# Kernel optimization log

Hardware: AMD Instinct MI355X
Metric: run time of the kernel (lower is better)

The kernel has to match this reference:

```python
import jax, jax.numpy as jnp
import numpy as np

N, SEQ_LEN, HORIZON, F_IN, EMBED, HIDDEN, LAYERS = 4096, 168, 24, 32, 32, 64, 2
G4 = 4 * HIDDEN
# NOTE: original torch code calls nn.LSTM per-step WITHOUT carrying hidden state,
# so each step's LSTM starts from (h0=0, c0=0): W_hh contributes nothing, only b_hh.

def setup_inputs() -> dict:
    key = jax.random.key(0)
    ks = jax.random.split(key, 12)
    s = 0.1
    return {
        "X": jax.random.normal(ks[0], (N, SEQ_LEN, F_IN), jnp.float32),
        "y": jax.random.normal(ks[1], (N, SEQ_LEN), jnp.float32),
        "Xf": jax.random.normal(ks[2], (N, HORIZON, F_IN), jnp.float32),
        "W_embed": jax.random.normal(ks[3], (EMBED, 1), jnp.float32) * s,
        "b_embed": jax.random.normal(ks[4], (EMBED,), jnp.float32) * s,
        "W_ih": jax.random.normal(ks[5], (LAYERS, G4, EMBED + F_IN), jnp.float32) * s,  # layer1 in-dim == HIDDEN == EMBED+F_IN
        "b_ih": jax.random.normal(ks[6], (LAYERS, G4), jnp.float32) * s,
        "b_hh": jax.random.normal(ks[7], (LAYERS, G4), jnp.float32) * s,
        "W_mu": jax.random.normal(ks[8], (1, HIDDEN), jnp.float32) * s,
        "b_mu": jax.random.normal(ks[9], (1,), jnp.float32) * s,
        "W_sigma": jax.random.normal(ks[10], (1, HIDDEN), jnp.float32) * s,
        "b_sigma": jax.random.normal(ks[11], (1,), jnp.float32) * s,
    }


def reference(X, y, Xf, W_embed, b_embed, W_ih, b_ih, b_hh, W_mu, b_mu, W_sigma, b_sigma):
    num_ts = X.shape[0]
    T = SEQ_LEN + HORIZON
    Xall = jnp.concatenate([X, Xf], axis=1)  # (N, T, F_IN)
    y_pad = jnp.concatenate([y, jnp.zeros((num_ts, HORIZON), y.dtype)], axis=1)  # (N, T)
    use_y = jnp.arange(T) < SEQ_LEN  # teacher-forced region

    def step(carry, inputs):
        x_s, y_s, use = inputs  # (N, F_IN), (N,), scalar bool
        ynext = jnp.where(use, y_s[:, None], carry)  # (N, 1)
        yembed = ynext @ W_embed.T + b_embed  # (N, EMBED)
        h = jnp.concatenate([x_s, yembed], axis=1)  # (N, F_IN+EMBED)
        for l in range(LAYERS):  # single LSTM step from zero state per layer
            gates = h @ W_ih[l].T + b_ih[l] + b_hh[l]  # (N, 4H); torch gate order i,f,g,o
            i_g, f_g, g_g, o_g = jnp.split(gates, 4, axis=1)
            c = jax.nn.sigmoid(i_g) * jnp.tanh(g_g)  # f * c0 term vanishes (c0 = 0)
            h = jax.nn.sigmoid(o_g) * jnp.tanh(c)
        h = jax.nn.relu(h)
        mu = h @ W_mu.T + b_mu  # (N, 1)
        sigma = jax.nn.softplus(h @ W_sigma.T + b_sigma) + 1e-6  # log(1+exp(.)) + eps
        lik = (2.0 * np.pi * sigma ** 2) ** (-0.5) * jnp.exp(-((ynext - mu) ** 2) / (2.0 * sigma ** 2))
        return lik, (lik[:, 0], mu[:, 0], sigma[:, 0])

    carry0 = jnp.zeros((num_ts, 1), X.dtype)
    xs = (jnp.swapaxes(Xall, 0, 1), y_pad.T, use_y)
    _, (lik_t, mu_t, sigma_t) = jax.lax.scan(step, carry0, xs)  # each (T, N)
    ypred = lik_t.T[:, SEQ_LEN - 1: SEQ_LEN + HORIZON - 1]  # (N, HORIZON)
    return ypred, mu_t.T, sigma_t.T
```

## Files before the change

### kernel.cpp

```cpp
#include <hip/hip_runtime.h>
#include <math.h>

#define N_TS 4096
#define SEQ  168
#define HOR  24
#define T_ALL 192
#define F_INP 32
#define HID  64
#define NROW 192
#define NB_B (N_TS / 32)
#define NT_B ((N_TS * SEQ) / 128)
#define L2E  1.44269504089f
#define W16F_L1 6144

typedef _Float16 half8  __attribute__((ext_vector_type(8)));
typedef _Float16 half4  __attribute__((ext_vector_type(4)));
typedef float    floatx4 __attribute__((ext_vector_type(4)));

__device__ __forceinline__ float fexp(float x)  { return __expf(x); }
__device__ __forceinline__ float ex2(float x)   { return __builtin_amdgcn_exp2f(x); }
__device__ __forceinline__ float frcp(float x)  { return __builtin_amdgcn_rcpf(x); }
__device__ __forceinline__ float softplus_(float x) { return (x > 15.0f) ? x : __logf(1.0f + fexp(x)); }

__device__ __forceinline__ float lstm_h(float ip, float gp, float op) {
    const float Ei = ex2(ip);
    const float Eg = ex2(gp);
    const float cc = (1.0f - Eg) * frcp((1.0f + Ei) * (1.0f + Eg));
    const float Ec = ex2(cc * (-2.0f * L2E));
    const float Eo = ex2(op);
    return (1.0f - Ec) * frcp((1.0f + Ec) * (1.0f + Eo));
}

__device__ __forceinline__ half8 cvt8(const float4 a, const float4 b) {
    half8 v;
    v[0]=(_Float16)a.x; v[1]=(_Float16)a.y; v[2]=(_Float16)a.z; v[3]=(_Float16)a.w;
    v[4]=(_Float16)b.x; v[5]=(_Float16)b.y; v[6]=(_Float16)b.z; v[7]=(_Float16)b.w;
    return v;
}

__global__ __launch_bounds__(256) void prep(
    const float* __restrict__ W_ih, const float* __restrict__ b_ih,
    const float* __restrict__ b_hh,
    const float* __restrict__ W_embed, const float* __restrict__ b_embed,
    _Float16* __restrict__ W16f, float* __restrict__ bsum,
    float* __restrict__ wy1, float* __restrict__ b1c)
{
    const int idx = blockIdx.x * 256 + threadIdx.x;
    for (int i = idx; i < 4 * NROW * 8; i += gridDim.x * 256) {
        const int kp  = i & 7;
        const int row = (i >> 3) % NROW;
        const int kb  = (i >> 3) / NROW;
        const int sr  = (row < 64) ? row : row + 64;
        const float sc = (row >= 64 && row < 128) ? (-2.0f * L2E) : (-L2E);
        W16f[i] = (_Float16)(W_ih[sr * HID + kb * 8 + kp] * sc);
    }
    for (int i = idx; i < 8 * NROW * 8; i += gridDim.x * 256) {
        const int kp  = i & 7;
        const int row = (i >> 3) % NROW;
        const int kb  = (i >> 3) / NROW;
        const int sr  = (row < 64) ? row : row + 64;
        const float sc = (row >= 64 && row < 128) ? (-2.0f * L2E) : (-L2E);
        W16f[W16F_L1 + i] = (_Float16)(W_ih[(256 + sr) * HID + kb * 8 + kp] * sc);
    }
    for (int i = idx; i < 2 * NROW; i += gridDim.x * 256) {
        const int r = i % NROW;
        const int l = i / NROW;
        const int sr = (r < 64) ? r : r + 64;
        const float sc = (r >= 64 && r < 128) ? (-2.0f * L2E) : (-L2E);
        bsum[i] = (b_ih[l * 256 + sr] + b_hh[l * 256 + sr]) * sc;
    }
    if (idx < NROW) {
        const int sr = (idx < 64) ? idx : idx + 64;
        const float sc = (idx >= 64 && idx < 128) ? (-2.0f * L2E) : (-L2E);
        const float* wrow = W_ih + sr * HID + 32;
        float s1 = 0.f, s2 = 0.f;
        #pragma unroll
        for (int k = 0; k < 32; ++k) {
            s1 = fmaf(wrow[k], W_embed[k], s1);
            s2 = fmaf(wrow[k], b_embed[k], s2);
        }
        wy1[idx] = s1 * sc;
        b1c[idx] = (b_ih[sr] + b_hh[sr] + s2) * sc;
    }
}

__global__ __launch_bounds__(512, 8) void fused(
    const float* __restrict__ X,
    const float* __restrict__ y,
    const float* __restrict__ Xf,
    const float* __restrict__ W_embed,
    const float* __restrict__ b_embed,
    const _Float16* __restrict__ W16f,
    const float* __restrict__ bsum,
    const float* __restrict__ wy1,
    const float* __restrict__ b1c,
    const float* __restrict__ W_mu,
    const float* __restrict__ b_mu,
    const float* __restrict__ W_sigma,
    const float* __restrict__ b_sigma,
    float* __restrict__ out)
{
    __shared__ union __align__(16) {
        struct { _Float16 Wl[12288]; _Float16 Hx[8][1024]; } A;
        struct { _Float16 slab[2][1024]; float partm[2][16][4]; float parts[2][16][4];
                 float wyb[NROW]; float b1cb[NROW]; } B;
    } sh;

    const int tid = threadIdx.x;
    float* mu_out = out + (size_t)N_TS * HOR;
    float* sg_out = mu_out + (size_t)N_TS * T_ALL;

    if (blockIdx.x < NB_B) {
        __builtin_amdgcn_s_setprio(1);
        const int w    = tid >> 6;
        const int g    = w >> 2;
        const int wg   = w & 3;
        const int lane = tid & 63;
        const int quad = lane >> 4;
        const int ln   = lane & 15;
        const int n0   = blockIdx.x * 32 + g * 16;

        if (tid < NROW) {
            sh.B.wyb[tid]  = wy1[tid];
            sh.B.b1cb[tid] = b1c[tid];
        }

        half8 B1[3];
        half8 B2[3][2];
        float bias2[3];
        #pragma unroll
        for (int j = 0; j < 3; ++j) {
            const int rt = j * 4 + wg;
            B1[j] = *(const half8*)(W16f + ((size_t)quad * NROW + rt * 16 + ln) * 8);
            #pragma unroll
            for (int kt = 0; kt < 2; ++kt)
                B2[j][kt] = *(const half8*)(W16f + W16F_L1 + ((size_t)(kt * 4 + quad) * NROW + rt * 16 + ln) * 8);
            bias2[j] = bsum[NROW + rt * 16 + ln];
        }
        const float wmu = W_mu[wg * 16 + ln], wsg = W_sigma[wg * 16 + ln];
        const float bmu = b_mu[0], bsg = b_sigma[0];

        const float* xfp = Xf + (size_t)(n0 + ln) * HOR * F_INP + quad * 8;
        float4 xa, xb;
        {
            const float* xp = X + ((size_t)(n0 + ln) * SEQ + (SEQ - 1)) * F_INP + quad * 8;
            xa = *(const float4*)xp;
            xb = *(const float4*)(xp + 4);
        }
        float ycur = y[(size_t)(n0 + ln) * SEQ + (SEQ - 1)];
        __syncthreads();

        #pragma unroll 1
        for (int it = 0; it <= HOR + 1; ++it) {
            if (it > 0) {
                const int k = it - 1;
                const float4 m4 = *(const float4*)sh.B.partm[g][ln];
                const float4 s4 = *(const float4*)sh.B.parts[g][ln];
                const float mu = (m4.x + m4.y) + (m4.z + m4.w) + bmu;
                const float sg = softplus_((s4.x + s4.y) + (s4.z + s4.w) + bsg) + 1e-6f;
                const float d  = ycur - mu;
                const float is = frcp(sg);
                const float lik = 0.39894228040143267f * is * fexp(-0.5f * d * d * is * is);
                if (k > 0 && wg == 0 && quad == 0) {
                    const int nn = n0 + ln;
                    const int t  = SEQ + k - 1;
                    mu_out[(size_t)nn * T_ALL + t] = mu;
                    sg_out[(size_t)nn * T_ALL + t] = sg;
                    if (k < HOR) out[(size_t)nn * HOR + k] = lik;
                }
                ycur = lik;
            }
            if (it > HOR) break;

            const half8 xf0 = cvt8(xa, xb);
            if (it < HOR) {
                xa = *(const float4*)(xfp + it * F_INP);
                xb = *(const float4*)(xfp + it * F_INP + 4);
            }

            floatx4 t0 = *(const floatx4*)(sh.B.b1cb + 0 * 64 + wg * 16 + quad * 4);
            floatx4 t1 = *(const floatx4*)(sh.B.b1cb + 1 * 64 + wg * 16 + quad * 4);
            floatx4 t2 = *(const floatx4*)(sh.B.b1cb + 2 * 64 + wg * 16 + quad * 4);
            t0 = __builtin_amdgcn_mfma_f32_16x16x32_f16(B1[0], xf0, t0, 0, 0, 0);
            t1 = __builtin_amdgcn_mfma_f32_16x16x32_f16(B1[1], xf0, t1, 0, 0, 0);
            t2 = __builtin_amdgcn_mfma_f32_16x16x32_f16(B1[2], xf0, t2, 0, 0, 0);

            const floatx4 wy0  = *(const floatx4*)(sh.B.wyb + 0 * 64 + wg * 16 + quad * 4);
            const floatx4 wy1v = *(const floatx4*)(sh.B.wyb + 1 * 64 + wg * 16 + quad * 4);
            const floatx4 wy2  = *(const floatx4*)(sh.B.wyb + 2 * 64 + wg * 16 + quad * 4);

            half4 h1p;
            #pragma unroll
            for (int r = 0; r < 4; ++r) {
                const float ig = fmaf(ycur, wy0[r],  t0[r]);
                const float gg = fmaf(ycur, wy1v[r], t1[r]);
                const float og = fmaf(ycur, wy2[r],  t2[r]);
                h1p[r] = (_Float16)lstm_h(ig, gg, og);
            }
            {
                const int xblk = (2 * wg + (quad >> 1)) ^ (ln & 7);
                *(half4*)(&sh.B.slab[g][ln * 64 + xblk * 8 + (quad & 1) * 4]) = h1p;
            }
            __syncthreads();

            const half8 a0 = *(const half8*)(&sh.B.slab[g][ln * 64 + ((quad ^ (ln & 7)) << 3)]);
            const half8 a1 = *(const half8*)(&sh.B.slab[g][ln * 64 + (((4 + quad) ^ (ln & 7)) << 3)]);
            floatx4 acc[3];
            #pragma unroll
            for (int j = 0; j < 3; ++j) {
                acc[j] = (floatx4){bias2[j], bias2[j], bias2[j], bias2[j]};
                acc[j] = __builtin_amdgcn_mfma_f32_16x16x32_f16(a0, B2[j][0], acc[j], 0, 0, 0);
                acc[j] = __builtin_amdgcn_mfma_f32_16x16x32_f16(a1, B2[j][1], acc[j], 0, 0, 0);
            }

            float pmr[4], psr[4];
            #pragma unroll
            for (int r = 0; r < 4; ++r) {
                const float hh = lstm_h(acc[0][r], acc[1][r], acc[2][r]);
                const float hr = fmaxf(hh, 0.0f);
                pmr[r] = hr * wmu;
                psr[r] = hr * wsg;
            }
            #pragma unroll
            for (int off = 1; off < 16; off <<= 1) {
                #pragma unroll
                for (int r = 0; r < 4; ++r) {
                    pmr[r] += __shfl_xor(pmr[r], off, 64);
                    psr[r] += __shfl_xor(psr[r], off, 64);
                }
            }
            if (ln == 0) {
                #pragma unroll
                for (int r = 0; r < 4; ++r) {
                    sh.B.partm[g][quad * 4 + r][wg] = pmr[r];
                    sh.B.parts[g][quad * 4 + r][wg] = psr[r];
                }
            }
            __syncthreads();
        }
        return;
    }

    const int w    = tid >> 6;
    const int lane = tid & 63;
    const int quad = lane >> 4;
    const int ln   = lane & 15;
    const int cid0 = (blockIdx.x - NB_B) * 128 + w * 16;
    const int cid  = cid0 + ln;

    half8 xfr;
    {
        const float* xp = X + (size_t)cid * F_INP + quad * 8;
        xfr = cvt8(*(const float4*)xp, *(const float4*)(xp + 4));
    }
    const float yv = y[cid];

    *(half8*)(sh.A.Wl + (size_t)tid * 8) = *(const half8*)(W16f + (size_t)tid * 8);
    if (tid < 256)
        *(half8*)(sh.A.Wl + (size_t)(512 + tid) * 8) = *(const half8*)(W16f + (size_t)(512 + tid) * 8);
    __syncthreads();

    _Float16* hrow = sh.A.Hx[w];
    {
        const _Float16* bp = sh.A.Wl + quad * 1536 + ln * 8;
        #pragma unroll
        for (int jt = 0; jt < 4; ++jt) {
            floatx4 ai = *(const floatx4*)(b1c + jt * 16 + quad * 4);
            floatx4 ag = *(const floatx4*)(b1c + 64 + jt * 16 + quad * 4);
            floatx4 ao = *(const floatx4*)(b1c + 128 + jt * 16 + quad * 4);
            ai = __builtin_amdgcn_mfma_f32_16x16x32_f16(*(const half8*)(bp + jt * 128),        xfr, ai, 0, 0, 0);
            ag = __builtin_amdgcn_mfma_f32_16x16x32_f16(*(const half8*)(bp + 512 + jt * 128),  xfr, ag, 0, 0, 0);
            ao = __builtin_amdgcn_mfma_f32_16x16x32_f16(*(const half8*)(bp + 1024 + jt * 128), xfr, ao, 0, 0, 0);
            const floatx4 wyi = *(const floatx4*)(wy1 + jt * 16 + quad * 4);
            const floatx4 wyg = *(const floatx4*)(wy1 + 64 + jt * 16 + quad * 4);
            const floatx4 wyo = *(const floatx4*)(wy1 + 128 + jt * 16 + quad * 4);
            half4 h1p;
            #pragma unroll
            for (int r = 0; r < 4; ++r) {
                h1p[r] = (_Float16)lstm_h(fmaf(yv, wyi[r], ai[r]),
                                          fmaf(yv, wyg[r], ag[r]),
                                          fmaf(yv, wyo[r], ao[r]));
            }
            const int xblk = (jt * 2 + (quad >> 1)) ^ (ln & 7);
            *(half4*)(&hrow[ln * 64 + xblk * 8 + (quad & 1) * 4]) = h1p;
        }
    }
    const half8 a0 = *(const half8*)(hrow + ln * 64 + ((quad ^ (ln & 7)) << 3));
    const half8 a1 = *(const half8*)(hrow + ln * 64 + (((4 + quad) ^ (ln & 7)) << 3));

    __syncthreads();
    *(half8*)(sh.A.Wl + (size_t)tid * 8)          = *(const half8*)(W16f + W16F_L1 + (size_t)tid * 8);
    *(half8*)(sh.A.Wl + (size_t)(512 + tid) * 8)  = *(const half8*)(W16f + W16F_L1 + (size_t)(512 + tid) * 8);
    *(half8*)(sh.A.Wl + (size_t)(1024 + tid) * 8) = *(const half8*)(W16f + W16F_L1 + (size_t)(1024 + tid) * 8);
    __syncthreads();

    float pm = 0.f, ps = 0.f;
    {
        const _Float16* bp = sh.A.Wl + quad * 1536 + ln * 8;
        #pragma unroll
        for (int jt = 0; jt < 4; ++jt) {
            floatx4 ai = *(const floatx4*)(bsum + NROW + jt * 16 + quad * 4);
            floatx4 ag = *(const floatx4*)(bsum + NROW + 64 + jt * 16 + quad * 4);
            floatx4 ao = *(const floatx4*)(bsum + NROW + 128 + jt * 16 + quad * 4);
            ai = __builtin_amdgcn_mfma_f32_16x16x32_f16(*(const half8*)(bp + jt * 128),               a0, ai, 0, 0, 0);
            ai = __builtin_amdgcn_mfma_f32_16x16x32_f16(*(const half8*)(bp + 6144 + jt * 128),        a1, ai, 0, 0, 0);
            ag = __builtin_amdgcn_mfma_f32_16x16x32_f16(*(const half8*)(bp + 512 + jt * 128),         a0, ag, 0, 0, 0);
            ag = __builtin_amdgcn_mfma_f32_16x16x32_f16(*(const half8*)(bp + 6144 + 512 + jt * 128),  a1, ag, 0, 0, 0);
            ao = __builtin_amdgcn_mfma_f32_16x16x32_f16(*(const half8*)(bp + 1024 + jt * 128),        a0, ao, 0, 0, 0);
            ao = __builtin_amdgcn_mfma_f32_16x16x32_f16(*(const half8*)(bp + 6144 + 1024 + jt * 128), a1, ao, 0, 0, 0);
            const floatx4 wm  = *(const floatx4*)(W_mu + jt * 16 + quad * 4);
            const floatx4 ws4 = *(const floatx4*)(W_sigma + jt * 16 + quad * 4);
            #pragma unroll
            for (int r = 0; r < 4; ++r) {
                const float hr = fmaxf(lstm_h(ai[r], ag[r], ao[r]), 0.0f);
                pm = fmaf(hr, wm[r], pm);
                ps = fmaf(hr, ws4[r], ps);
            }
        }
    }
    pm += __shfl_xor(pm, 16, 64); pm += __shfl_xor(pm, 32, 64);
    ps += __shfl_xor(ps, 16, 64); ps += __shfl_xor(ps, 32, 64);

    if (quad == 0) {
        const int n = cid / SEQ;
        const int t = cid - n * SEQ;
        const float mu = pm + b_mu[0];
        const float sg = softplus_(ps + b_sigma[0]) + 1e-6f;
        mu_out[(size_t)n * T_ALL + t] = mu;
        sg_out[(size_t)n * T_ALL + t] = sg;
        if (t == SEQ - 1) {
            const float d  = yv - mu;
            const float is = frcp(sg);
            out[(size_t)n * HOR] = 0.39894228040143267f * is * fexp(-0.5f * d * d * is * is);
        }
    }
}

extern "C" void kernel_launch(void* const* d_in, const int* in_sizes, int n_in,
                              void* d_out, int out_size, void* d_ws, size_t ws_size,
                              hipStream_t stream) {
    const float* X       = (const float*)d_in[0];
    const float* y       = (const float*)d_in[1];
    const float* Xf      = (const float*)d_in[2];
    const float* W_embed = (const float*)d_in[3];
    const float* b_embed = (const float*)d_in[4];
    const float* W_ih    = (const float*)d_in[5];
    const float* b_ih    = (const float*)d_in[6];
    const float* b_hh    = (const float*)d_in[7];
    const float* W_mu    = (const float*)d_in[8];
    const float* b_mu    = (const float*)d_in[9];
    const float* W_sigma = (const float*)d_in[10];
    const float* b_sigma = (const float*)d_in[11];

    float* out = (float*)d_out;
    _Float16*  W16f = (_Float16*)d_ws;
    float*     bsum = (float*)((char*)d_ws + 36864);
    float*     wy1  = (float*)((char*)d_ws + 36864 + 1536);
    float*     b1c  = (float*)((char*)d_ws + 36864 + 1536 + 768);

    prep<<<96, 256, 0, stream>>>(W_ih, b_ih, b_hh, W_embed, b_embed,
                                 W16f, bsum, wy1, b1c);

    fused<<<NB_B + NT_B, 512, 0, stream>>>(
        X, y, Xf, W_embed, b_embed, W16f, bsum, wy1, b1c,
        W_mu, b_mu, W_sigma, b_sigma, out);
}
```

Measured before the change: 276.0 us.

## Keep layer-1 hidden state in registers via permuted weights and halve block size

Prep writes a second copy of the layer-2 weights with the K dimension permuted to match the MFMA output layout. The teacher-forced path can then pack layer-1 outputs straight into the A operands in registers, skipping the per-wave shared-memory Hx staging and its write/read round trip. Blocks shrink from 512 to 256 threads: the autoregressive path handles 16 series per block instead of 32, and the teacher-forced path handles 64 rows per block. This shrinks the LDS footprint and changes occupancy, at the cost of more blocks and repeated weight staging per block.

New measurement: 252.4 us. -8.6%, faster.

```diff
diff --git a/kernel.cpp b/kernel.cpp
--- a/kernel.cpp
+++ b/kernel.cpp
@@ -8,10 +8,11 @@
 #define F_INP 32
 #define HID  64
 #define NROW 192
-#define NB_B (N_TS / 32)
-#define NT_B ((N_TS * SEQ) / 128)
+#define NB_B (N_TS / 16)
+#define NT_B ((N_TS * SEQ) / 64)
 #define L2E  1.44269504089f
-#define W16F_L1 6144
+#define W16F_L1  6144
+#define W16F_L1P 18432
 
 typedef _Float16 half8  __attribute__((ext_vector_type(8)));
 typedef _Float16 half4  __attribute__((ext_vector_type(4)));
@@ -62,6 +63,20 @@
         const float sc = (row >= 64 && row < 128) ? (-2.0f * L2E) : (-L2E);
         W16f[W16F_L1 + i] = (_Float16)(W_ih[(256 + sr) * HID + kb * 8 + kp] * sc);
     }
+    for (int i = idx; i < 8 * NROW * 8; i += gridDim.x * 256) {
+        const int kp  = i & 7;
+        const int row = (i >> 3) % NROW;
+        const int kb  = (i >> 3) / NROW;
+        const int k   = kb * 8 + kp;
+        const int kk  = k & 31;
+        const int d   = (kk >> 1) & 3;
+        const int q   = kk >> 3;
+        const int e   = kk & 1;
+        const int hid = d * 16 + q * 4 + ((k >> 5) << 1) + e;
+        const int sr  = (row < 64) ? row : row + 64;
+        const float sc = (row >= 64 && row < 128) ? (-2.0f * L2E) : (-L2E);
+        W16f[W16F_L1P + i] = (_Float16)(W_ih[(256 + sr) * HID + hid] * sc);
+    }
     for (int i = idx; i < 2 * NROW; i += gridDim.x * 256) {
         const int r = i % NROW;
         const int l = i / NROW;
@@ -84,7 +99,7 @@
     }
 }
 
-__global__ __launch_bounds__(512, 8) void fused(
+__global__ __launch_bounds__(256, 6) void fused(
     const float* __restrict__ X,
     const float* __restrict__ y,
     const float* __restrict__ Xf,
@@ -101,8 +116,8 @@
     float* __restrict__ out)
 {
     __shared__ union __align__(16) {
-        struct { _Float16 Wl[12288]; _Float16 Hx[8][1024]; } A;
-        struct { _Float16 slab[2][1024]; float partm[2][16][4]; float parts[2][16][4];
+        struct { _Float16 Wl[12288]; } A;
+        struct { _Float16 slab[16 * 64]; float partm[16][4]; float parts[16][4];
                  float wyb[NROW]; float b1cb[NROW]; } B;
     } sh;
 
@@ -113,12 +128,10 @@
     if (blockIdx.x < NB_B) {
         __builtin_amdgcn_s_setprio(1);
         const int w    = tid >> 6;
-        const int g    = w >> 2;
-        const int wg   = w & 3;
         const int lane = tid & 63;
         const int quad = lane >> 4;
         const int ln   = lane & 15;
-        const int n0   = blockIdx.x * 32 + g * 16;
+        const int n0   = blockIdx.x * 16;
 
         if (tid < NROW) {
             sh.B.wyb[tid]  = wy1[tid];
@@ -130,14 +143,14 @@
         float bias2[3];
         #pragma unroll
         for (int j = 0; j < 3; ++j) {
-            const int rt = j * 4 + wg;
+            const int rt = j * 4 + w;
             B1[j] = *(const half8*)(W16f + ((size_t)quad * NROW + rt * 16 + ln) * 8);
             #pragma unroll
             for (int kt = 0; kt < 2; ++kt)
                 B2[j][kt] = *(const half8*)(W16f + W16F_L1 + ((size_t)(kt * 4 + quad) * NROW + rt * 16 + ln) * 8);
             bias2[j] = bsum[NROW + rt * 16 + ln];
         }
-        const float wmu = W_mu[wg * 16 + ln], wsg = W_sigma[wg * 16 + ln];
+        const float wmu = W_mu[w * 16 + ln], wsg = W_sigma[w * 16 + ln];
         const float bmu = b_mu[0], bsg = b_sigma[0];
 
         const float* xfp = Xf + (size_t)(n0 + ln) * HOR * F_INP + quad * 8;
@@ -154,14 +167,14 @@
         for (int it = 0; it <= HOR + 1; ++it) {
             if (it > 0) {
                 const int k = it - 1;
-                const float4 m4 = *(const float4*)sh.B.partm[g][ln];
-                const float4 s4 = *(const float4*)sh.B.parts[g][ln];
+                const float4 m4 = *(const float4*)sh.B.partm[ln];
+                const float4 s4 = *(const float4*)sh.B.parts[ln];
                 const float mu = (m4.x + m4.y) + (m4.z + m4.w) + bmu;
                 const float sg = softplus_((s4.x + s4.y) + (s4.z + s4.w) + bsg) + 1e-6f;
                 const float d  = ycur - mu;
                 const float is = frcp(sg);
                 const float lik = 0.39894228040143267f * is * fexp(-0.5f * d * d * is * is);
-                if (k > 0 && wg == 0 && quad == 0) {
+                if (k > 0 && w == 0 && quad == 0) {
                     const int nn = n0 + ln;
                     const int t  = SEQ + k - 1;
                     mu_out[(size_t)nn * T_ALL + t] = mu;
@@ -178,16 +191,16 @@
                 xb = *(const float4*)(xfp + it * F_INP + 4);
             }
 
-            floatx4 t0 = *(const floatx4*)(sh.B.b1cb + 0 * 64 + wg * 16 + quad * 4);
-            floatx4 t1 = *(const floatx4*)(sh.B.b1cb + 1 * 64 + wg * 16 + quad * 4);
-            floatx4 t2 = *(const floatx4*)(sh.B.b1cb + 2 * 64 + wg * 16 + quad * 4);
+            floatx4 t0 = *(const floatx4*)(sh.B.b1cb + 0 * 64 + w * 16 + quad * 4);
+            floatx4 t1 = *(const floatx4*)(sh.B.b1cb + 1 * 64 + w * 16 + quad * 4);
+            floatx4 t2 = *(const floatx4*)(sh.B.b1cb + 2 * 64 + w * 16 + quad * 4);
             t0 = __builtin_amdgcn_mfma_f32_16x16x32_f16(B1[0], xf0, t0, 0, 0, 0);
             t1 = __builtin_amdgcn_mfma_f32_16x16x32_f16(B1[1], xf0, t1, 0, 0, 0);
             t2 = __builtin_amdgcn_mfma_f32_16x16x32_f16(B1[2], xf0, t2, 0, 0, 0);
 
-            const floatx4 wy0  = *(const floatx4*)(sh.B.wyb + 0 * 64 + wg * 16 + quad * 4);
-            const floatx4 wy1v = *(const floatx4*)(sh.B.wyb + 1 * 64 + wg * 16 + quad * 4);
-            const floatx4 wy2  = *(const floatx4*)(sh.B.wyb + 2 * 64 + wg * 16 + quad * 4);
+            const floatx4 wy0  = *(const floatx4*)(sh.B.wyb + 0 * 64 + w * 16 + quad * 4);
+            const floatx4 wy1v = *(const floatx4*)(sh.B.wyb + 1 * 64 + w * 16 + quad * 4);
+            const floatx4 wy2  = *(const floatx4*)(sh.B.wyb + 2 * 64 + w * 16 + quad * 4);
 
             half4 h1p;
             #pragma unroll
@@ -198,13 +211,13 @@
                 h1p[r] = (_Float16)lstm_h(ig, gg, og);
             }
             {
-                const int xblk = (2 * wg + (quad >> 1)) ^ (ln & 7);
-                *(half4*)(&sh.B.slab[g][ln * 64 + xblk * 8 + (quad & 1) * 4]) = h1p;
+                const int xblk = (2 * w + (quad >> 1)) ^ (ln & 7);
+                *(half4*)(&sh.B.slab[ln * 64 + xblk * 8 + (quad & 1) * 4]) = h1p;
             }
             __syncthreads();
 
-            const half8 a0 = *(const half8*)(&sh.B.slab[g][ln * 64 + ((quad ^ (ln & 7)) << 3)]);
-            const half8 a1 = *(const half8*)(&sh.B.slab[g][ln * 64 + (((4 + quad) ^ (ln & 7)) << 3)]);
+            const half8 a0 = *(const half8*)(&sh.B.slab[ln * 64 + ((quad ^ (ln & 7)) << 3)]);
+            const half8 a1 = *(const half8*)(&sh.B.slab[ln * 64 + (((4 + quad) ^ (ln & 7)) << 3)]);
             floatx4 acc[3];
             #pragma unroll
             for (int j = 0; j < 3; ++j) {
@@ -232,8 +245,8 @@
             if (ln == 0) {
                 #pragma unroll
                 for (int r = 0; r < 4; ++r) {
-                    sh.B.partm[g][quad * 4 + r][wg] = pmr[r];
-                    sh.B.parts[g][quad * 4 + r][wg] = psr[r];
+                    sh.B.partm[quad * 4 + r][w] = pmr[r];
+                    sh.B.parts[quad * 4 + r][w] = psr[r];
                 }
             }
             __syncthreads();
@@ -245,8 +258,7 @@
     const int lane = tid & 63;
     const int quad = lane >> 4;
     const int ln   = lane & 15;
-    const int cid0 = (blockIdx.x - NB_B) * 128 + w * 16;
-    const int cid  = cid0 + ln;
+    const int cid  = (blockIdx.x - NB_B) * 64 + w * 16 + ln;
 
     half8 xfr;
     {
@@ -255,12 +267,14 @@
     }
     const float yv = y[cid];
 
-    *(half8*)(sh.A.Wl + (size_t)tid * 8) = *(const half8*)(W16f + (size_t)tid * 8);
-    if (tid < 256)
-        *(half8*)(sh.A.Wl + (size_t)(512 + tid) * 8) = *(const half8*)(W16f + (size_t)(512 + tid) * 8);
+    #pragma unroll
+    for (int c = 0; c < 3; ++c) {
+        const int off = (c * 256 + tid) * 8;
+        *(half8*)(sh.A.Wl + off) = *(const half8*)(W16f + off);
+    }
     __syncthreads();
 
-    _Float16* hrow = sh.A.Hx[w];
+    half8 a0, a1;
     {
         const _Float16* bp = sh.A.Wl + quad * 1536 + ln * 8;
         #pragma unroll
@@ -274,24 +288,27 @@
             const floatx4 wyi = *(const floatx4*)(wy1 + jt * 16 + quad * 4);
             const floatx4 wyg = *(const floatx4*)(wy1 + 64 + jt * 16 + quad * 4);
             const floatx4 wyo = *(const floatx4*)(wy1 + 128 + jt * 16 + quad * 4);
-            half4 h1p;
-            #pragma unroll
-            for (int r = 0; r < 4; ++r) {
-                h1p[r] = (_Float16)lstm_h(fmaf(yv, wyi[r], ai[r]),
-                                          fmaf(yv, wyg[r], ag[r]),
-                                          fmaf(yv, wyo[r], ao[r]));
-            }
-            const int xblk = (jt * 2 + (quad >> 1)) ^ (ln & 7);
-            *(half4*)(&hrow[ln * 64 + xblk * 8 + (quad & 1) * 4]) = h1p;
-        }
-    }
-    const half8 a0 = *(const half8*)(hrow + ln * 64 + ((quad ^ (ln & 7)) << 3));
-    const half8 a1 = *(const half8*)(hrow + ln * 64 + (((4 + quad) ^ (ln & 7)) << 3));
+            a0[2 * jt + 0] = (_Float16)lstm_h(fmaf(yv, wyi[0], ai[0]),
+                                              fmaf(yv, wyg[0], ag[0]),
+                                              fmaf(yv, wyo[0], ao[0]));
+            a0[2 * jt + 1] = (_Float16)lstm_h(fmaf(yv, wyi[1], ai[1]),
+                                              fmaf(yv, wyg[1], ag[1]),
+                                              fmaf(yv, wyo[1], ao[1]));
+            a1[2 * jt + 0] = (_Float16)lstm_h(fmaf(yv, wyi[2], ai[2]),
+                                              fmaf(yv, wyg[2], ag[2]),
+                                              fmaf(yv, wyo[2], ao[2]));
+            a1[2 * jt + 1] = (_Float16)lstm_h(fmaf(yv, wyi[3], ai[3]),
+                                              fmaf(yv, wyg[3], ag[3]),
+                                              fmaf(yv, wyo[3], ao[3]));
+        }
+    }
 
     __syncthreads();
-    *(half8*)(sh.A.Wl + (size_t)tid * 8)          = *(const half8*)(W16f + W16F_L1 + (size_t)tid * 8);
-    *(half8*)(sh.A.Wl + (size_t)(512 + tid) * 8)  = *(const half8*)(W16f + W16F_L1 + (size_t)(512 + tid) * 8);
-    *(half8*)(sh.A.Wl + (size_t)(1024 + tid) * 8) = *(const half8*)(W16f + W16F_L1 + (size_t)(1024 + tid) * 8);
+    #pragma unroll
+    for (int c = 0; c < 6; ++c) {
+        const int off = (c * 256 + tid) * 8;
+        *(half8*)(sh.A.Wl + off) = *(const half8*)(W16f + W16F_L1P + off);
+    }
     __syncthreads();
 
     float pm = 0.f, ps = 0.f;
@@ -354,14 +371,14 @@
 
     float* out = (float*)d_out;
     _Float16*  W16f = (_Float16*)d_ws;
-    float*     bsum = (float*)((char*)d_ws + 36864);
-    float*     wy1  = (float*)((char*)d_ws + 36864 + 1536);
-    float*     b1c  = (float*)((char*)d_ws + 36864 + 1536 + 768);
+    float*     bsum = (float*)((char*)d_ws + 61440);
+    float*     wy1  = (float*)((char*)d_ws + 61440 + 1536);
+    float*     b1c  = (float*)((char*)d_ws + 61440 + 1536 + 768);
 
     prep<<<96, 256, 0, stream>>>(W_ih, b_ih, b_hh, W_embed, b_embed,
                                  W16f, bsum, wy1, b1c);
 
-    fused<<<NB_B + NT_B, 512, 0, stream>>>(
+    fused<<<NB_B + NT_B, 256, 0, stream>>>(
         X, y, Xf, W_embed, b_embed, W16f, bsum, wy1, b1c,
         W_mu, b_mu, W_sigma, b_sigma, out);
 }
```
